# Optimization experiments

Measured on AMD Instinct MI355X. Metric: run time of the kernel, lower is better.

## Reference

```python
import jax, jax.numpy as jnp
import numpy as np
from jax import lax

K = 3
LRELU_SLOPE = 0.2
GAIN = float(np.sqrt(2.0))


def setup_inputs() -> dict:
    key = jax.random.key(0)
    ks = jax.random.split(key, 7)
    B, Cin, Cout, H, W, S = 8, 64, 64, 256, 256, 512
    return {
        "x": jax.random.normal(ks[0], (B, Cin, H, W), dtype=jnp.float32),
        "style": jax.random.normal(ks[1], (B, S), dtype=jnp.float32),
        "noise": jax.random.normal(ks[2], (B, 1, H, W), dtype=jnp.float32),
        "weight": jax.random.normal(ks[3], (Cout, Cin, K, K), dtype=jnp.float32),
        "mod_w": jax.random.normal(ks[4], (S, Cin), dtype=jnp.float32),
        "mod_b": jnp.ones((Cin,), dtype=jnp.float32),
        "noise_weight": jax.random.uniform(ks[5], (1,), dtype=jnp.float32),
        "bias": jax.random.normal(ks[6], (Cout,), dtype=jnp.float32),
    }


def _styled_conv(x, style, noise, weight, mod_w, mod_b, noise_weight, bias):
    B, Cin, H, W = x.shape
    Cout = weight.shape[0]
    S = mod_w.shape[0]
    conv_scale = 1.0 / jnp.sqrt(jnp.float32(Cin * K * K))
    lin_scale = 1.0 / jnp.sqrt(jnp.float32(S))
    # EqualLinear modulation: [B, Cin]
    s = style @ (mod_w * lin_scale) + mod_b
    # per-sample modulated weights: [B, Cout, Cin, K, K]
    w = conv_scale * weight[None] * s[:, None, :, None, None]
    # demodulation over (Cin, K, K)
    demod = lax.rsqrt(jnp.sum(w * w, axis=(2, 3, 4)) + 1e-8)  # [B, Cout]
    w = w * demod[:, :, None, None, None]

    def conv_one(xi, wi):  # xi: [Cin,H,W], wi: [Cout,Cin,K,K]
        return lax.conv_general_dilated(
            xi[None], wi, window_strides=(1, 1),
            padding=[(K // 2, K // 2), (K // 2, K // 2)],
            dimension_numbers=("NCHW", "OIHW", "NCHW"))[0]

    out = jax.vmap(conv_one)(x, w)  # [B, Cout, H, W]
    out = out + noise_weight[0] * noise  # noise broadcast over channels
    out = jax.nn.leaky_relu(out + bias[None, :, None, None], LRELU_SLOPE) * GAIN
    return out


def reference(x, style, noise, weight, mod_w, mod_b, noise_weight, bias):
    return _styled_conv(x, style, noise, weight, mod_w, mod_b, noise_weight, bias)
```

## Files before the change

kernel.cpp:

```cpp
#include <hip/hip_runtime.h>
#include <hip/hip_bf16.h>

#define BB   8
#define CC   64
#define HH   256
#define WW   256
#define SS   512
#define HW   (HH*WW)

#define LIN_SCALE  0.044194173824159216f
#define CONV_SCALE 0.041666666666666664f
#define LRELU      0.2f
#define GAIN       1.4142135623730951f

#define TY 8
#define TX 32
#define LY (TY + 2)
#define LX (TX + 2)

typedef __attribute__((ext_vector_type(8)))  short short8;
typedef __attribute__((ext_vector_type(16))) float floatx16;

static __device__ __forceinline__ unsigned short f2bf(float f) {
    unsigned u = __float_as_uint(f);
    u += 0x7FFF + ((u >> 16) & 1);
    return (unsigned short)(u >> 16);
}

static __device__ __forceinline__ unsigned pk2(float a, float b) {
    __hip_bfloat162 h = __float22bfloat162_rn(make_float2(a, b));
    return *(unsigned*)&h;
}

#define VC(vv,kk) ((kk)==0?(vv).x:((kk)==1?(vv).y:((kk)==2?(vv).z:(vv).w)))

__global__ void mod_kernel(const float* __restrict__ style,
                           const float* __restrict__ mod_w,
                           const float* __restrict__ mod_b,
                           float* __restrict__ s_out) {
    __shared__ float part[256];
    int b = blockIdx.x;
    int t = threadIdx.x;
    int ci = t & 63, kp = t >> 6;
    const float* st = style + b * SS + kp * 128;
    float acc = 0.f;
    for (int k = 0; k < 128; ++k)
        acc = fmaf(st[k], mod_w[(kp * 128 + k) * CC + ci], acc);
    part[t] = acc;
    __syncthreads();
    if (t < 64) {
        float v = part[t] + part[t + 64] + part[t + 128] + part[t + 192];
        s_out[b * CC + t] = v * LIN_SCALE + mod_b[t];
    }
}

__global__ void wmod_kernel(const float* __restrict__ weight,
                            const float* __restrict__ s_in,
                            unsigned short* __restrict__ wbf) {
    int bc = blockIdx.x;
    int b = bc >> 6, co = bc & 63;
    int ci = threadIdx.x;
    float wv[9];
    float sv = s_in[b * CC + ci] * CONV_SCALE;
    float sum = 0.f;
    const float* wp = weight + (co * CC + ci) * 9;
#pragma unroll
    for (int k = 0; k < 9; ++k) {
        wv[k] = wp[k] * sv;
        sum = fmaf(wv[k], wv[k], sum);
    }
#pragma unroll
    for (int off = 32; off; off >>= 1)
        sum += __shfl_xor(sum, off);
    float demod = rsqrtf(sum + 1e-8f);
    int g = ci >> 3, j = ci & 7;
#pragma unroll
    for (int ko = 0; ko < 9; ++ko) {
        size_t idx = ((((size_t)b * 9 + ko) * 8 + g) * 64 + co) * 8 + j;
        wbf[idx] = f2bf(wv[ko] * demod);
    }
}

__global__ __launch_bounds__(256, 2) void conv_kernel(
        const float* __restrict__ x,
        const float* __restrict__ noise,
        const float* __restrict__ nwp,
        const float* __restrict__ bias,
        const unsigned short* __restrict__ wbf,
        float* __restrict__ out) {
    extern __shared__ unsigned short smem[];
    unsigned short* xs   = smem;
    unsigned short* wlds = smem + 8 * LY * LX * 8;

    const int lin  = blockIdx.x;
    const int lin2 = (lin & 7) * 256 + (lin >> 3);
    const int b   = lin2 >> 8;
    const int rem = lin2 & 255;
    const int by  = rem >> 3;
    const int bx  = rem & 7;
    const int x0t = bx * TX;
    const int y0t = by * TY;

    const int t = threadIdx.x;
    const int lane = t & 63;
    const int wv = t >> 6;
    const int n31 = lane & 31;
    const int h   = lane >> 5;

#pragma unroll
    for (int it = 0; it < 4; ++it) {
        int n = t + it * 256;
        n = n < 799 ? n : 799;
        int q = n % 10;
        int rest = n / 10;
        int yl = rest % 10;
        int g  = rest / 10;
        int gy = y0t + yl - 1;
        int gx0 = x0t - 4 + q * 4;
        bool rowok = (unsigned)gy < (unsigned)HH;
        int gyc  = gy < 0 ? 0 : (gy > HH - 1 ? HH - 1 : gy);
        int gx0c = gx0 < 0 ? 0 : (gx0 > WW - 4 ? WW - 4 : gx0);
        const float* xp = x + ((size_t)b * CC + g * 8) * HW + (size_t)gyc * WW + gx0c;
        float4 v[8];
#pragma unroll
        for (int j = 0; j < 8; ++j)
            v[j] = *(const float4*)(xp + (size_t)j * HW);
#pragma unroll
        for (int k = 0; k < 4; ++k) {
            int lx = 4 * q - 3 + k;
            if ((unsigned)lx < (unsigned)LX) {
                bool ok = rowok && ((unsigned)(gx0 + k) < (unsigned)WW);
                uint4 w;
                w.x = ok ? pk2(VC(v[0], k), VC(v[1], k)) : 0u;
                w.y = ok ? pk2(VC(v[2], k), VC(v[3], k)) : 0u;
                w.z = ok ? pk2(VC(v[4], k), VC(v[5], k)) : 0u;
                w.w = ok ? pk2(VC(v[6], k), VC(v[7], k)) : 0u;
                *(uint4*)&xs[((g * LY + yl) * LX + lx) * 8] = w;
            }
        }
    }

    floatx16 acc[2][2];
    acc[0][0] = (floatx16)0.f; acc[0][1] = (floatx16)0.f;
    acc[1][0] = (floatx16)0.f; acc[1][1] = (floatx16)0.f;

#pragma unroll 1
    for (int kh = 0; kh < 3; ++kh) {
        __syncthreads();
        {
            const unsigned short* wsrc = wbf + ((size_t)b * 9 + kh * 3) * 4096;
#pragma unroll
            for (int i = 0; i < 6; ++i) {
                int idx = t + i * 256;
                *(uint4*)&wlds[idx * 8] = *(const uint4*)&wsrc[idx * 8];
            }
        }
        __syncthreads();

#pragma unroll
        for (int kw = 0; kw < 3; ++kw) {
#pragma unroll
            for (int kc = 0; kc < 4; ++kc) {
                const int g = kc * 2 + h;
                short8 av0 = *(const short8*)&wlds[((kw * 8 + g) * 64 + n31) * 8];
                short8 av1 = *(const short8*)&wlds[((kw * 8 + g) * 64 + 32 + n31) * 8];
#pragma unroll
                for (int rl = 0; rl < 2; ++rl) {
                    int ys = wv * 2 + rl + kh;
                    short8 bv = *(const short8*)&xs[((g * LY + ys) * LX + kw + n31) * 8];
                    acc[rl][0] = __builtin_amdgcn_mfma_f32_32x32x16_bf16(
                        av0, bv, acc[rl][0], 0, 0, 0);
                    acc[rl][1] = __builtin_amdgcn_mfma_f32_32x32x16_bf16(
                        av1, bv, acc[rl][1], 0, 0, 0);
                }
            }
        }
    }

    float nw = nwp[0];
    float bv0[16], bv1[16];
#pragma unroll
    for (int reg = 0; reg < 16; ++reg) {
        int cr = (reg & 3) + 8 * (reg >> 2) + 4 * h;
        bv0[reg] = bias[cr];
        bv1[reg] = bias[32 + cr];
    }

#pragma unroll
    for (int rl = 0; rl < 2; ++rl) {
        int py = y0t + wv * 2 + rl;
        float nz = nw * noise[(size_t)b * HW + (size_t)py * WW + x0t + n31];
#pragma unroll
        for (int reg = 0; reg < 16; ++reg) {
            int cr = (reg & 3) + 8 * (reg >> 2) + 4 * h;
            float v0 = acc[rl][0][reg] + nz + bv0[reg];
            v0 = (v0 > 0.f ? v0 : LRELU * v0) * GAIN;
            out[((size_t)b * CC + cr) * HW + (size_t)py * WW + x0t + n31] = v0;
            float v1 = acc[rl][1][reg] + nz + bv1[reg];
            v1 = (v1 > 0.f ? v1 : LRELU * v1) * GAIN;
            out[((size_t)b * CC + 32 + cr) * HW + (size_t)py * WW + x0t + n31] = v1;
        }
    }
}

extern "C" void kernel_launch(void* const* d_in, const int* in_sizes, int n_in,
                              void* d_out, int out_size, void* d_ws, size_t ws_size,
                              hipStream_t stream) {
    const float* x       = (const float*)d_in[0];
    const float* style   = (const float*)d_in[1];
    const float* noise   = (const float*)d_in[2];
    const float* weight  = (const float*)d_in[3];
    const float* mod_w   = (const float*)d_in[4];
    const float* mod_b   = (const float*)d_in[5];
    const float* nw      = (const float*)d_in[6];
    const float* bias    = (const float*)d_in[7];
    float* out = (float*)d_out;

    float* s_buf          = (float*)d_ws;
    unsigned short* wbf   = (unsigned short*)((char*)d_ws + 4096);

    mod_kernel<<<dim3(BB), dim3(256), 0, stream>>>(style, mod_w, mod_b, s_buf);
    wmod_kernel<<<dim3(BB * CC), dim3(CC), 0, stream>>>(weight, s_buf, wbf);
    const int lds_bytes = (8 * LY * LX * 8 + 3 * 8 * 64 * 8) * 2;
    conv_kernel<<<dim3((WW / TX) * (HH / TY) * BB), dim3(256), lds_bytes, stream>>>(
        x, noise, nw, bias, wbf, out);
}
```

Measured before the change: 95.00 us.

## Make conv kernel persistent with double-buffered input tiles and resident weights

Each conv block now handles eight consecutive row tiles instead of one, with 256 blocks total. All nine weight taps are loaded into LDS once per block. The next input tile's global loads are issued into registers before the MFMA loop and written to a second LDS buffer afterwards, so load latency overlaps compute. The cost is lower occupancy (launch bounds drop to one block per SM), more LDS and many more live registers, and only 256 blocks to spread across the GPU.

```diff
diff --git a/kernel.cpp b/kernel.cpp
--- a/kernel.cpp
+++ b/kernel.cpp
@@ -17,6 +17,8 @@
 #define TX 32
 #define LY (TY + 2)
 #define LX (TX + 2)
+#define XSE (8 * LY * LX * 8)
+#define WLE (9 * 8 * 64 * 8)
 
 typedef __attribute__((ext_vector_type(8)))  short short8;
 typedef __attribute__((ext_vector_type(16))) float floatx16;
@@ -81,7 +83,7 @@
     }
 }
 
-__global__ __launch_bounds__(256, 2) void conv_kernel(
+__global__ __launch_bounds__(256, 1) void conv_kernel(
         const float* __restrict__ x,
         const float* __restrict__ noise,
         const float* __restrict__ nwp,
@@ -89,17 +91,17 @@
         const unsigned short* __restrict__ wbf,
         float* __restrict__ out) {
     extern __shared__ unsigned short smem[];
-    unsigned short* xs   = smem;
-    unsigned short* wlds = smem + 8 * LY * LX * 8;
+    unsigned short* xsA  = smem;
+    unsigned short* xsB  = smem + XSE;
+    unsigned short* wlds = smem + 2 * XSE;
 
     const int lin  = blockIdx.x;
-    const int lin2 = (lin & 7) * 256 + (lin >> 3);
-    const int b   = lin2 >> 8;
-    const int rem = lin2 & 255;
-    const int by  = rem >> 3;
+    const int lin2 = (lin & 7) * 32 + (lin >> 3);
+    const int b   = lin2 >> 5;
+    const int rem = lin2 & 31;
     const int bx  = rem & 7;
+    const int sy  = rem >> 3;
     const int x0t = bx * TX;
-    const int y0t = by * TY;
 
     const int t = threadIdx.x;
     const int lane = t & 63;
@@ -107,67 +109,110 @@
     const int n31 = lane & 31;
     const int h   = lane >> 5;
 
-#pragma unroll
-    for (int it = 0; it < 4; ++it) {
-        int n = t + it * 256;
-        n = n < 799 ? n : 799;
-        int q = n % 10;
-        int rest = n / 10;
-        int yl = rest % 10;
-        int g  = rest / 10;
-        int gy = y0t + yl - 1;
-        int gx0 = x0t - 4 + q * 4;
-        bool rowok = (unsigned)gy < (unsigned)HH;
-        int gyc  = gy < 0 ? 0 : (gy > HH - 1 ? HH - 1 : gy);
-        int gx0c = gx0 < 0 ? 0 : (gx0 > WW - 4 ? WW - 4 : gx0);
-        const float* xp = x + ((size_t)b * CC + g * 8) * HW + (size_t)gyc * WW + gx0c;
-        float4 v[8];
-#pragma unroll
-        for (int j = 0; j < 8; ++j)
-            v[j] = *(const float4*)(xp + (size_t)j * HW);
-#pragma unroll
-        for (int k = 0; k < 4; ++k) {
-            int lx = 4 * q - 3 + k;
-            if ((unsigned)lx < (unsigned)LX) {
-                bool ok = rowok && ((unsigned)(gx0 + k) < (unsigned)WW);
-                uint4 w;
-                w.x = ok ? pk2(VC(v[0], k), VC(v[1], k)) : 0u;
-                w.y = ok ? pk2(VC(v[2], k), VC(v[3], k)) : 0u;
-                w.z = ok ? pk2(VC(v[4], k), VC(v[5], k)) : 0u;
-                w.w = ok ? pk2(VC(v[6], k), VC(v[7], k)) : 0u;
-                *(uint4*)&xs[((g * LY + yl) * LX + lx) * 8] = w;
-            }
-        }
-    }
-
-    floatx16 acc[2][2];
-    acc[0][0] = (floatx16)0.f; acc[0][1] = (floatx16)0.f;
-    acc[1][0] = (floatx16)0.f; acc[1][1] = (floatx16)0.f;
+    const float nw = nwp[0];
+
+    {
+        const uint4* wsrc = (const uint4*)(wbf + (size_t)b * WLE);
+        uint4* wdst = (uint4*)wlds;
+#pragma unroll
+        for (int i = 0; i < 18; ++i)
+            wdst[t + i * 256] = wsrc[t + i * 256];
+    }
+
+    float4 vreg[4][8];
+    {
+        const int y0n = sy * 64;
+#pragma unroll
+        for (int it = 0; it < 4; ++it) {
+            int n = t + it * 256; n = n < 799 ? n : 799;
+            int q = n % 10; int rest = n / 10;
+            int yl = rest % 10; int g = rest / 10;
+            int gy = y0n + yl - 1;
+            int gx0 = x0t - 4 + q * 4;
+            int gyc  = gy < 0 ? 0 : (gy > HH - 1 ? HH - 1 : gy);
+            int gx0c = gx0 < 0 ? 0 : (gx0 > WW - 4 ? WW - 4 : gx0);
+            const float* xp = x + ((size_t)b * CC + g * 8) * HW + (size_t)gyc * WW + gx0c;
+#pragma unroll
+            for (int j = 0; j < 8; ++j)
+                vreg[it][j] = *(const float4*)(xp + (size_t)j * HW);
+        }
+#pragma unroll
+        for (int it = 0; it < 4; ++it) {
+            int n = t + it * 256; n = n < 799 ? n : 799;
+            int q = n % 10; int rest = n / 10;
+            int yl = rest % 10; int g = rest / 10;
+            int gy = y0n + yl - 1;
+            int gx0 = x0t - 4 + q * 4;
+            bool rowok = (unsigned)gy < (unsigned)HH;
+#pragma unroll
+            for (int k = 0; k < 4; ++k) {
+                int lx = 4 * q - 3 + k;
+                if ((unsigned)lx < (unsigned)LX) {
+                    bool ok = rowok && ((unsigned)(gx0 + k) < (unsigned)WW);
+                    uint4 w;
+                    w.x = ok ? pk2(VC(vreg[it][0], k), VC(vreg[it][1], k)) : 0u;
+                    w.y = ok ? pk2(VC(vreg[it][2], k), VC(vreg[it][3], k)) : 0u;
+                    w.z = ok ? pk2(VC(vreg[it][4], k), VC(vreg[it][5], k)) : 0u;
+                    w.w = ok ? pk2(VC(vreg[it][6], k), VC(vreg[it][7], k)) : 0u;
+                    *(uint4*)&xsA[((g * LY + yl) * LX + lx) * 8] = w;
+                }
+            }
+        }
+    }
+    float nzc0, nzc1;
+    {
+        int py0 = sy * 64 + wv * 2;
+        nzc0 = noise[(size_t)b * HW + (size_t)py0 * WW + x0t + n31];
+        nzc1 = noise[(size_t)b * HW + (size_t)(py0 + 1) * WW + x0t + n31];
+    }
+    __syncthreads();
+
+    unsigned short* xcur = xsA;
+    unsigned short* xnxt = xsB;
 
 #pragma unroll 1
-    for (int kh = 0; kh < 3; ++kh) {
-        __syncthreads();
-        {
-            const unsigned short* wsrc = wbf + ((size_t)b * 9 + kh * 3) * 4096;
-#pragma unroll
-            for (int i = 0; i < 6; ++i) {
-                int idx = t + i * 256;
-                *(uint4*)&wlds[idx * 8] = *(const uint4*)&wsrc[idx * 8];
-            }
-        }
-        __syncthreads();
-
-#pragma unroll
-        for (int kw = 0; kw < 3; ++kw) {
+    for (int tt = 0; tt < 8; ++tt) {
+        const int y0t = (sy * 8 + tt) * TY;
+        float nzn0 = 0.f, nzn1 = 0.f;
+
+        if (tt < 7) {
+            const int y0n = y0t + TY;
+#pragma unroll
+            for (int it = 0; it < 4; ++it) {
+                int n = t + it * 256; n = n < 799 ? n : 799;
+                int q = n % 10; int rest = n / 10;
+                int yl = rest % 10; int g = rest / 10;
+                int gy = y0n + yl - 1;
+                int gx0 = x0t - 4 + q * 4;
+                int gyc  = gy < 0 ? 0 : (gy > HH - 1 ? HH - 1 : gy);
+                int gx0c = gx0 < 0 ? 0 : (gx0 > WW - 4 ? WW - 4 : gx0);
+                const float* xp = x + ((size_t)b * CC + g * 8) * HW + (size_t)gyc * WW + gx0c;
+#pragma unroll
+                for (int j = 0; j < 8; ++j)
+                    vreg[it][j] = *(const float4*)(xp + (size_t)j * HW);
+            }
+            int pyn = y0n + wv * 2;
+            nzn0 = noise[(size_t)b * HW + (size_t)pyn * WW + x0t + n31];
+            nzn1 = noise[(size_t)b * HW + (size_t)(pyn + 1) * WW + x0t + n31];
+        }
+        __builtin_amdgcn_sched_barrier(0);
+
+        floatx16 acc[2][2];
+        acc[0][0] = (floatx16)0.f; acc[0][1] = (floatx16)0.f;
+        acc[1][0] = (floatx16)0.f; acc[1][1] = (floatx16)0.f;
+
+#pragma unroll
+        for (int ko = 0; ko < 9; ++ko) {
+            const int kh = ko / 3, kw = ko % 3;
 #pragma unroll
             for (int kc = 0; kc < 4; ++kc) {
                 const int g = kc * 2 + h;
-                short8 av0 = *(const short8*)&wlds[((kw * 8 + g) * 64 + n31) * 8];
-                short8 av1 = *(const short8*)&wlds[((kw * 8 + g) * 64 + 32 + n31) * 8];
+                short8 av0 = *(const short8*)&wlds[((ko * 8 + g) * 64 + n31) * 8];
+                short8 av1 = *(const short8*)&wlds[((ko * 8 + g) * 64 + 32 + n31) * 8];
 #pragma unroll
                 for (int rl = 0; rl < 2; ++rl) {
                     int ys = wv * 2 + rl + kh;
-                    short8 bv = *(const short8*)&xs[((g * LY + ys) * LX + kw + n31) * 8];
+                    short8 bv = *(const short8*)&xcur[((g * LY + ys) * LX + kw + n31) * 8];
                     acc[rl][0] = __builtin_amdgcn_mfma_f32_32x32x16_bf16(
                         av0, bv, acc[rl][0], 0, 0, 0);
                     acc[rl][1] = __builtin_amdgcn_mfma_f32_32x32x16_bf16(
@@ -175,31 +220,56 @@
                 }
             }
         }
-    }
-
-    float nw = nwp[0];
-    float bv0[16], bv1[16];
-#pragma unroll
-    for (int reg = 0; reg < 16; ++reg) {
-        int cr = (reg & 3) + 8 * (reg >> 2) + 4 * h;
-        bv0[reg] = bias[cr];
-        bv1[reg] = bias[32 + cr];
-    }
-
-#pragma unroll
-    for (int rl = 0; rl < 2; ++rl) {
-        int py = y0t + wv * 2 + rl;
-        float nz = nw * noise[(size_t)b * HW + (size_t)py * WW + x0t + n31];
-#pragma unroll
-        for (int reg = 0; reg < 16; ++reg) {
-            int cr = (reg & 3) + 8 * (reg >> 2) + 4 * h;
-            float v0 = acc[rl][0][reg] + nz + bv0[reg];
-            v0 = (v0 > 0.f ? v0 : LRELU * v0) * GAIN;
-            out[((size_t)b * CC + cr) * HW + (size_t)py * WW + x0t + n31] = v0;
-            float v1 = acc[rl][1][reg] + nz + bv1[reg];
-            v1 = (v1 > 0.f ? v1 : LRELU * v1) * GAIN;
-            out[((size_t)b * CC + 32 + cr) * HW + (size_t)py * WW + x0t + n31] = v1;
-        }
+        __builtin_amdgcn_sched_barrier(0);
+
+        if (tt < 7) {
+            const int y0n = y0t + TY;
+#pragma unroll
+            for (int it = 0; it < 4; ++it) {
+                int n = t + it * 256; n = n < 799 ? n : 799;
+                int q = n % 10; int rest = n / 10;
+                int yl = rest % 10; int g = rest / 10;
+                int gy = y0n + yl - 1;
+                int gx0 = x0t - 4 + q * 4;
+                bool rowok = (unsigned)gy < (unsigned)HH;
+#pragma unroll
+                for (int k = 0; k < 4; ++k) {
+                    int lx = 4 * q - 3 + k;
+                    if ((unsigned)lx < (unsigned)LX) {
+                        bool ok = rowok && ((unsigned)(gx0 + k) < (unsigned)WW);
+                        uint4 w;
+                        w.x = ok ? pk2(VC(vreg[it][0], k), VC(vreg[it][1], k)) : 0u;
+                        w.y = ok ? pk2(VC(vreg[it][2], k), VC(vreg[it][3], k)) : 0u;
+                        w.z = ok ? pk2(VC(vreg[it][4], k), VC(vreg[it][5], k)) : 0u;
+                        w.w = ok ? pk2(VC(vreg[it][6], k), VC(vreg[it][7], k)) : 0u;
+                        *(uint4*)&xnxt[((g * LY + yl) * LX + lx) * 8] = w;
+                    }
+                }
+            }
+        }
+
+        {
+            float nz0 = nw * nzc0, nz1 = nw * nzc1;
+#pragma unroll
+            for (int rl = 0; rl < 2; ++rl) {
+                int py = y0t + wv * 2 + rl;
+                float nz = rl ? nz1 : nz0;
+#pragma unroll
+                for (int reg = 0; reg < 16; ++reg) {
+                    int cr = (reg & 3) + 8 * (reg >> 2) + 4 * h;
+                    float v0 = acc[rl][0][reg] + nz + bias[cr];
+                    v0 = (v0 > 0.f ? v0 : LRELU * v0) * GAIN;
+                    out[((size_t)b * CC + cr) * HW + (size_t)py * WW + x0t + n31] = v0;
+                    float v1 = acc[rl][1][reg] + nz + bias[32 + cr];
+                    v1 = (v1 > 0.f ? v1 : LRELU * v1) * GAIN;
+                    out[((size_t)b * CC + 32 + cr) * HW + (size_t)py * WW + x0t + n31] = v1;
+                }
+            }
+        }
+
+        __syncthreads();
+        unsigned short* tmp = xcur; xcur = xnxt; xnxt = tmp;
+        nzc0 = nzn0; nzc1 = nzn1;
     }
 }
 
@@ -221,7 +291,7 @@
 
     mod_kernel<<<dim3(BB), dim3(256), 0, stream>>>(style, mod_w, mod_b, s_buf);
     wmod_kernel<<<dim3(BB * CC), dim3(CC), 0, stream>>>(weight, s_buf, wbf);
-    const int lds_bytes = (8 * LY * LX * 8 + 3 * 8 * 64 * 8) * 2;
-    conv_kernel<<<dim3((WW / TX) * (HH / TY) * BB), dim3(256), lds_bytes, stream>>>(
+    const int lds_bytes = (2 * XSE + WLE) * 2;
+    conv_kernel<<<dim3(256), dim3(256), lds_bytes, stream>>>(
         x, noise, nw, bias, wbf, out);
 }
```

New measurement: 114.5 us. 1.21x slower.

## Load modulated weights directly from global into registers with prefetch, drop LDS staging

Applied to the files above, without the earlier changes.

The conv kernel no longer stages the per-sample modulated weights through LDS in three kh phases with barriers. Each lane now reads its MFMA A-operand fragments straight from global memory (L2-resident) and prefetches the next fragment one step ahead. This removes two barriers per kh and shrinks LDS to only the input tile, and launch bounds are raised to allow three blocks per CU. The trade-off is more global/L2 traffic for weights, since each wave re-reads them, plus higher register pressure from the prefetch under a tighter occupancy target.

```diff
diff --git a/kernel.cpp b/kernel.cpp
--- a/kernel.cpp
+++ b/kernel.cpp
@@ -17,6 +17,7 @@
 #define TX 32
 #define LY (TY + 2)
 #define LX (TX + 2)
+#define WLE (9 * 8 * 64 * 8)
 
 typedef __attribute__((ext_vector_type(8)))  short short8;
 typedef __attribute__((ext_vector_type(16))) float floatx16;
@@ -81,16 +82,14 @@
     }
 }
 
-__global__ __launch_bounds__(256, 2) void conv_kernel(
+__global__ __launch_bounds__(256, 3) void conv_kernel(
         const float* __restrict__ x,
         const float* __restrict__ noise,
         const float* __restrict__ nwp,
         const float* __restrict__ bias,
         const unsigned short* __restrict__ wbf,
         float* __restrict__ out) {
-    extern __shared__ unsigned short smem[];
-    unsigned short* xs   = smem;
-    unsigned short* wlds = smem + 8 * LY * LX * 8;
+    __shared__ unsigned short xs[8 * LY * LX * 8];
 
     const int lin  = blockIdx.x;
     const int lin2 = (lin & 7) * 256 + (lin >> 3);
@@ -139,53 +138,47 @@
             }
         }
     }
+    __syncthreads();
+
+    const unsigned short* wb = wbf + (size_t)b * WLE;
+#define ALOAD(ko, kc, m) \
+    (*(const short8*)&wb[((((ko) * 8 + (kc) * 2 + h) * 64) + (m) * 32 + n31) * 8])
 
     floatx16 acc[2][2];
     acc[0][0] = (floatx16)0.f; acc[0][1] = (floatx16)0.f;
     acc[1][0] = (floatx16)0.f; acc[1][1] = (floatx16)0.f;
 
-#pragma unroll 1
-    for (int kh = 0; kh < 3; ++kh) {
-        __syncthreads();
-        {
-            const unsigned short* wsrc = wbf + ((size_t)b * 9 + kh * 3) * 4096;
-#pragma unroll
-            for (int i = 0; i < 6; ++i) {
-                int idx = t + i * 256;
-                *(uint4*)&wlds[idx * 8] = *(const uint4*)&wsrc[idx * 8];
+    short8 a0 = ALOAD(0, 0, 0);
+    short8 a1 = ALOAD(0, 0, 1);
+
+#pragma unroll
+    for (int ko = 0; ko < 9; ++ko) {
+        const int kh = ko / 3, kw = ko % 3;
+#pragma unroll
+        for (int kc = 0; kc < 4; ++kc) {
+            short8 p0 = a0, p1 = a1;
+            if (!(ko == 8 && kc == 3)) {
+                int nko = (kc == 3) ? ko + 1 : ko;
+                int nkc = (kc == 3) ? 0 : kc + 1;
+                p0 = ALOAD(nko, nkc, 0);
+                p1 = ALOAD(nko, nkc, 1);
             }
+            const int g = kc * 2 + h;
+#pragma unroll
+            for (int rl = 0; rl < 2; ++rl) {
+                int ys = wv * 2 + rl + kh;
+                short8 bv = *(const short8*)&xs[((g * LY + ys) * LX + kw + n31) * 8];
+                acc[rl][0] = __builtin_amdgcn_mfma_f32_32x32x16_bf16(
+                    a0, bv, acc[rl][0], 0, 0, 0);
+                acc[rl][1] = __builtin_amdgcn_mfma_f32_32x32x16_bf16(
+                    a1, bv, acc[rl][1], 0, 0, 0);
+            }
+            a0 = p0; a1 = p1;
         }
-        __syncthreads();
-
-#pragma unroll
-        for (int kw = 0; kw < 3; ++kw) {
-#pragma unroll
-            for (int kc = 0; kc < 4; ++kc) {
-                const int g = kc * 2 + h;
-                short8 av0 = *(const short8*)&wlds[((kw * 8 + g) * 64 + n31) * 8];
-                short8 av1 = *(const short8*)&wlds[((kw * 8 + g) * 64 + 32 + n31) * 8];
-#pragma unroll
-                for (int rl = 0; rl < 2; ++rl) {
-                    int ys = wv * 2 + rl + kh;
-                    short8 bv = *(const short8*)&xs[((g * LY + ys) * LX + kw + n31) * 8];
-                    acc[rl][0] = __builtin_amdgcn_mfma_f32_32x32x16_bf16(
-                        av0, bv, acc[rl][0], 0, 0, 0);
-                    acc[rl][1] = __builtin_amdgcn_mfma_f32_32x32x16_bf16(
-                        av1, bv, acc[rl][1], 0, 0, 0);
-                }
-            }
-        }
-    }
+    }
+#undef ALOAD
 
     float nw = nwp[0];
-    float bv0[16], bv1[16];
-#pragma unroll
-    for (int reg = 0; reg < 16; ++reg) {
-        int cr = (reg & 3) + 8 * (reg >> 2) + 4 * h;
-        bv0[reg] = bias[cr];
-        bv1[reg] = bias[32 + cr];
-    }
-
 #pragma unroll
     for (int rl = 0; rl < 2; ++rl) {
         int py = y0t + wv * 2 + rl;
@@ -193,10 +186,10 @@
 #pragma unroll
         for (int reg = 0; reg < 16; ++reg) {
             int cr = (reg & 3) + 8 * (reg >> 2) + 4 * h;
-            float v0 = acc[rl][0][reg] + nz + bv0[reg];
+            float v0 = acc[rl][0][reg] + nz + bias[cr];
             v0 = (v0 > 0.f ? v0 : LRELU * v0) * GAIN;
             out[((size_t)b * CC + cr) * HW + (size_t)py * WW + x0t + n31] = v0;
-            float v1 = acc[rl][1][reg] + nz + bv1[reg];
+            float v1 = acc[rl][1][reg] + nz + bias[32 + cr];
             v1 = (v1 > 0.f ? v1 : LRELU * v1) * GAIN;
             out[((size_t)b * CC + 32 + cr) * HW + (size_t)py * WW + x0t + n31] = v1;
         }
@@ -221,7 +214,6 @@
 
     mod_kernel<<<dim3(BB), dim3(256), 0, stream>>>(style, mod_w, mod_b, s_buf);
     wmod_kernel<<<dim3(BB * CC), dim3(CC), 0, stream>>>(weight, s_buf, wbf);
-    const int lds_bytes = (8 * LY * LX * 8 + 3 * 8 * 64 * 8) * 2;
-    conv_kernel<<<dim3((WW / TX) * (HH / TY) * BB), dim3(256), lds_bytes, stream>>>(
+    conv_kernel<<<dim3((WW / TX) * (HH / TY) * BB), dim3(256), 0, stream>>>(
         x, noise, nw, bias, wbf, out);
 }
```

After: 94.26 us. About the same (-0.8%).
